# Performance work log

Hardware: AMD Instinct MI355X
Metric: run time of the kernel (lower is better)

Reference implementation:

```python
import jax, jax.numpy as jnp
import numpy as np

R = 32
EPS = 0.0
BN_EPS = 1e-5


def _voxelize(features, idx):
    # features: [C, N], idx: [N] int32 flat voxel index in [0, R^3)
    V = R * R * R
    pts = features.T  # [N, C]
    sums = jax.ops.segment_sum(pts, idx, num_segments=V)          # [V, C]
    cnts = jax.ops.segment_sum(jnp.ones_like(idx, jnp.float32), idx, num_segments=V)  # [V]
    avg = sums / jnp.maximum(cnts, 1.0)[:, None]
    mx = jax.ops.segment_max(pts, idx, num_segments=V)            # [V, C], -inf for empty
    mx = jnp.where(cnts[:, None] > 0, mx, 0.0)
    return avg, mx, cnts


def reference(features, coords, conv_w, conv_b, bn_gamma, bn_beta, bn_mean, bn_var):
    B, C, N = features.shape
    # --- coordinate normalization (coords detached in original) ---
    nc = coords - jnp.mean(coords, axis=2, keepdims=True)          # [B,3,N]
    norms = jnp.linalg.norm(nc, axis=1, keepdims=True)             # [B,1,N]
    denom = jnp.max(norms, axis=2, keepdims=True) * 2.0 + EPS      # [B,1,1]
    nc = nc / denom + 0.5
    nc = jnp.clip(nc * R, 0.0, R - 1)                              # [B,3,N]
    vox = jnp.round(nc).astype(jnp.int32)                          # [B,3,N]
    idx = vox[:, 0] * (R * R) + vox[:, 1] * R + vox[:, 2]          # [B,N]
    # --- dual scatter reduction (avg + max) per batch ---
    avg, mx, _ = jax.vmap(_voxelize)(features, idx)                # [B, V, C] each
    fea = jnp.concatenate([mx, avg], axis=-1)                      # [B, V, 2C]
    # --- 1x1 Conv3d == channel matmul ---
    y = jnp.einsum('bvc,oc->bvo', fea, conv_w) + conv_b            # [B, V, C]
    # --- BatchNorm3d (eval mode) ---
    y = (y - bn_mean) * (bn_gamma / jnp.sqrt(bn_var + BN_EPS)) + bn_beta
    # --- Swish ---
    y = y * jax.nn.sigmoid(y)
    out = jnp.transpose(y, (0, 2, 1)).reshape(B, C, R, R, R)
    return out, nc


def setup_inputs() -> dict:
    key = jax.random.key(0)
    ks = jax.random.split(key, 8)
    B, C, N = 8, 240, 16384
    return {
        'features': jax.random.normal(ks[0], (B, C, N), jnp.float32),
        'coords': jax.random.normal(ks[1], (B, 3, N), jnp.float32),
        'conv_w': jax.random.normal(ks[2], (C, 2 * C), jnp.float32) * 0.05,
        'conv_b': jax.random.normal(ks[3], (C,), jnp.float32) * 0.05,
        'bn_gamma': jnp.ones((C,), jnp.float32),
        'bn_beta': jnp.zeros((C,), jnp.float32),
        'bn_mean': jnp.zeros((C,), jnp.float32),
        'bn_var': jax.random.uniform(ks[4], (C,), jnp.float32, 0.5, 1.5),
    }
```

## Files before the change

### kernel.cpp

```cpp
#include <hip/hip_runtime.h>
#include <math.h>

#define RR 32
#define V 32768
#define C 240
#define N 16384
#define B 8
#define K2C 480
#define NCOL 1024
#define FPAD 488
#define EBUF 512

typedef __attribute__((ext_vector_type(8))) short bf16x8;
typedef __attribute__((ext_vector_type(4))) float f32x4;

__device__ __forceinline__ unsigned short f2bf(float x) {
    unsigned u = __float_as_uint(x);
    u += 0x7fffu + ((u >> 16) & 1u);
    return (unsigned short)(u >> 16);
}
__device__ __forceinline__ float bf2f(unsigned short u) {
    return __uint_as_float(((unsigned)u) << 16);
}

__global__ __launch_bounds__(1024) void stats_kernel(const float* __restrict__ coords,
                                                     float* __restrict__ stats) {
    int b = blockIdx.x, tid = threadIdx.x;
    const float* cb = coords + (size_t)b * 3 * N;
    __shared__ float red[1024];
    float m[3];
    for (int d = 0; d < 3; ++d) {
        float s = 0.f;
        for (int n = tid; n < N; n += 1024) s += cb[d * N + n];
        red[tid] = s; __syncthreads();
        for (int w = 512; w > 0; w >>= 1) { if (tid < w) red[tid] += red[tid + w]; __syncthreads(); }
        m[d] = red[0] / (float)N;
        __syncthreads();
    }
    float mx = 0.f;
    for (int n = tid; n < N; n += 1024) {
        float dx = cb[0 * N + n] - m[0];
        float dy = cb[1 * N + n] - m[1];
        float dz = cb[2 * N + n] - m[2];
        mx = fmaxf(mx, dx * dx + dy * dy + dz * dz);
    }
    red[tid] = mx; __syncthreads();
    for (int w = 512; w > 0; w >>= 1) { if (tid < w) red[tid] = fmaxf(red[tid], red[tid + w]); __syncthreads(); }
    if (tid == 0) {
        stats[b * 4 + 0] = m[0];
        stats[b * 4 + 1] = m[1];
        stats[b * 4 + 2] = m[2];
        stats[b * 4 + 3] = 2.f * sqrtf(red[0]);
    }
}

__global__ __launch_bounds__(256) void nc_idx_kernel(const float* __restrict__ coords,
                                                     const float* __restrict__ stats,
                                                     float* __restrict__ nc_out,
                                                     int* __restrict__ idxbuf,
                                                     int* __restrict__ hist) {
    int t = blockIdx.x * 256 + threadIdx.x;
    int b = t >> 14;
    int n = t & (N - 1);
    float denom = stats[b * 4 + 3];
    int v[3];
#pragma unroll
    for (int d = 0; d < 3; ++d) {
        float x = coords[((size_t)b * 3 + d) * N + n];
        float t0 = (x - stats[b * 4 + d]) / denom + 0.5f;
        t0 = t0 * (float)RR;
        t0 = fminf(fmaxf(t0, 0.f), (float)(RR - 1));
        nc_out[((size_t)b * 3 + d) * N + n] = t0;
        v[d] = (int)rintf(t0);
    }
    int iv = v[0] * (RR * RR) + v[1] * RR + v[2];
    idxbuf[t] = iv;
    atomicAdd(hist + b * V + iv, 1);
}

__global__ __launch_bounds__(1024) void prefix_kernel(const int* __restrict__ hist,
                                                      int* __restrict__ starts,
                                                      int* __restrict__ cursor) {
    __shared__ int part[1024];
    int b = blockIdx.x, t = threadIdx.x;
    int base = b * V + t * 32;
    int s = 0;
    for (int j = 0; j < 32; ++j) s += hist[base + j];
    part[t] = s; __syncthreads();
    for (int off = 1; off < 1024; off <<= 1) {
        int x = (t >= off) ? part[t - off] : 0;
        __syncthreads();
        part[t] += x;
        __syncthreads();
    }
    int run = part[t] - s;
    for (int j = 0; j < 32; ++j) {
        int h = hist[base + j];
        starts[base + j] = run;
        cursor[base + j] = run;
        run += h;
    }
}

__global__ __launch_bounds__(256) void plist_kernel(const int* __restrict__ idxbuf,
                                                    int* __restrict__ cursor,
                                                    int* __restrict__ ptlist) {
    int t = blockIdx.x * 256 + threadIdx.x;
    int b = t >> 14;
    int n = t & (N - 1);
    int iv = idxbuf[t];
    int pos = atomicAdd(cursor + b * V + iv, 1);
    ptlist[(b << 14) + pos] = (n << 5) | (iv & 31);
}

__global__ __launch_bounds__(256) void wcvt_kernel(const float* __restrict__ w,
                                                   unsigned short* __restrict__ w_bf) {
    int i = blockIdx.x * 256 + threadIdx.x;
    w_bf[i] = f2bf(w[i]);
}

__global__ __launch_bounds__(256) void transpose_kernel(const float* __restrict__ feat,
                                                        unsigned short* __restrict__ featT) {
    __shared__ float t[32][33];
    int b = blockIdx.z;
    int n0 = blockIdx.x * 32, c0 = blockIdx.y * 32;
    int l = threadIdx.x;
    int tx = l & 31, ty = l >> 5;
    const float* fb = feat + (size_t)b * C * N;
    unsigned short* fTb = featT + (size_t)b * N * C;
#pragma unroll
    for (int k = 0; k < 4; ++k) {
        int c = c0 + ty + 8 * k;
        if (c < C) t[ty + 8 * k][tx] = fb[(size_t)c * N + n0 + tx];
    }
    __syncthreads();
    int cp = l & 15;
    int nl = l >> 4;
#pragma unroll
    for (int k = 0; k < 2; ++k) {
        int n = n0 + nl + 16 * k;
        int c = c0 + 2 * cp;
        if (c < C) {
            unsigned lo = f2bf(t[2 * cp][nl + 16 * k]);
            unsigned hi = f2bf(t[2 * cp + 1][nl + 16 * k]);
            *(unsigned*)&fTb[(size_t)n * C + c] = lo | (hi << 16);
        }
    }
}

__global__ __launch_bounds__(256) void column_kernel(
    const unsigned short* __restrict__ featT,
    const int* __restrict__ ptlist,
    const int* __restrict__ starts,
    const int* __restrict__ hist,
    const unsigned short* __restrict__ w_bf,
    const float* __restrict__ cbias, const float* __restrict__ gamma,
    const float* __restrict__ beta, const float* __restrict__ mean,
    const float* __restrict__ var,
    float* __restrict__ out) {
    const int col = blockIdx.x, b = blockIdx.y;
    const int tid = threadIdx.x;
    const int v0 = col * 32;
    float* outb = out + (size_t)b * C * V;

    __shared__ float A_s[C], B_s[C];
    __shared__ unsigned short fea_s[32][FPAD];
    __shared__ int cnt_s[32];
    __shared__ int ebuf[EBUF];

    if (tid < C) {
        float sc = gamma[tid] * rsqrtf(var[tid] + 1e-5f);
        A_s[tid] = sc;
        B_s[tid] = (cbias[tid] - mean[tid]) * sc + beta[tid];
    }
    if (tid < 32) cnt_s[tid] = hist[b * V + v0 + tid];
    __syncthreads();

    int pc = 0;
#pragma unroll
    for (int z = 0; z < 32; ++z) pc += cnt_s[z];

    if (pc == 0) {
        for (int i = tid; i < C * 32; i += 256) {
            int o = i >> 5, vv = i & 31;
            float y = B_s[o];
            y = y / (1.f + __expf(-y));
            outb[(size_t)o * V + v0 + vv] = y;
        }
        return;
    }

    for (int i = tid; i < 32 * FPAD / 2; i += 256) ((unsigned*)fea_s)[i] = 0u;

    const int c = (tid < C) ? tid : 0;
    const bool act = tid < C;
    const int pos = starts[b * V + v0];
    const int* pl = ptlist + (b << 14) + pos;
    const unsigned short* fT = featT + (size_t)b * N * C;

    float s = 0.f, mx = -INFINITY;
    int curz = -1;
    for (int base = 0; base < pc; base += EBUF) {
        int mm = min(EBUF, pc - base);
        __syncthreads();
        for (int i = tid; i < mm; i += 256) ebuf[i] = pl[base + i];
        __syncthreads();
        for (int i0 = 0; i0 < mm; i0 += 16) {
            int m = min(16, mm - i0);
            int e_[16];
#pragma unroll
            for (int j = 0; j < 16; ++j) e_[j] = ebuf[i0 + ((j < m) ? j : m - 1)];
            float f_[16];
#pragma unroll
            for (int j = 0; j < 16; ++j) f_[j] = bf2f(fT[(e_[j] >> 5) * C + c]);
#pragma unroll
            for (int j = 0; j < 16; ++j) {
                if (j < m) {
                    int zj = e_[j] & 31;
                    if (zj != curz) {
                        if (curz >= 0 && act) {
                            fea_s[curz][c] = f2bf(mx);
                            fea_s[curz][C + c] = f2bf(s / (float)cnt_s[curz]);
                        }
                        curz = zj; s = 0.f; mx = -INFINITY;
                    }
                    s += f_[j]; mx = fmaxf(mx, f_[j]);
                }
            }
        }
    }
    if (curz >= 0 && act) {
        fea_s[curz][c] = f2bf(mx);
        fea_s[curz][C + c] = f2bf(s / (float)cnt_s[curz]);
    }
    __syncthreads();

    const int lane = tid & 63, wave = tid >> 6;
    const int nt = wave & 1;
    const int mbase = (wave >> 1) * 8;
    const int mcnt = (wave >> 1) ? 7 : 8;
    const int zl = nt * 16 + (lane & 15);
    const int koff = (lane >> 4) * 8;

    f32x4 acc[8];
#pragma unroll
    for (int i = 0; i < 8; ++i) acc[i] = (f32x4){0.f, 0.f, 0.f, 0.f};

#pragma unroll
    for (int kc = 0; kc < 15; ++kc) {
        const int kg = kc * 32 + koff;
        bf16x8 bfr = *(const bf16x8*)&fea_s[zl][kg];
        const unsigned short* wp = w_bf + (size_t)(mbase * 16 + (lane & 15)) * K2C + kg;
#pragma unroll
        for (int mt = 0; mt < 8; ++mt) {
            if (mt < mcnt) {
                bf16x8 afr = *(const bf16x8*)(wp + (size_t)mt * 16 * K2C);
                acc[mt] = __builtin_amdgcn_mfma_f32_16x16x32_bf16(afr, bfr, acc[mt], 0, 0, 0);
            }
        }
    }

    const int vv = v0 + zl;
    const int rbase = (lane >> 4) * 4;
#pragma unroll
    for (int mt = 0; mt < 8; ++mt) {
        if (mt < mcnt) {
#pragma unroll
            for (int r = 0; r < 4; ++r) {
                int o = (mbase + mt) * 16 + rbase + r;
                float y = acc[mt][r] * A_s[o] + B_s[o];
                y = y / (1.f + __expf(-y));
                outb[(size_t)o * V + vv] = y;
            }
        }
    }
}

extern "C" void kernel_launch(void* const* d_in, const int* in_sizes, int n_in,
                              void* d_out, int out_size, void* d_ws, size_t ws_size,
                              hipStream_t stream) {
    const float* features = (const float*)d_in[0];
    const float* coords   = (const float*)d_in[1];
    const float* conv_w   = (const float*)d_in[2];
    const float* conv_b   = (const float*)d_in[3];
    const float* gamma    = (const float*)d_in[4];
    const float* beta     = (const float*)d_in[5];
    const float* mean     = (const float*)d_in[6];
    const float* var      = (const float*)d_in[7];

    float* out    = (float*)d_out;
    float* nc_out = out + (size_t)B * C * V;

    char* ws = (char*)d_ws;
    size_t off = 0;
    auto carve = [&](size_t bytes) { char* p = ws + off; off += (bytes + 255) & ~(size_t)255; return p; };
    int*            hist   = (int*)carve((size_t)B * V * 4);
    float*          stats  = (float*)carve(B * 4 * 4);
    int*            idxbuf = (int*)carve((size_t)B * N * 4);
    int*            starts = (int*)carve((size_t)B * V * 4);
    int*            cursor = (int*)carve((size_t)B * V * 4);
    int*            ptlist = (int*)carve((size_t)B * N * 4);
    unsigned short* w_bf   = (unsigned short*)carve((size_t)C * K2C * 2);
    unsigned short* featT  = (unsigned short*)carve((size_t)B * N * C * 2);
    (void)off;

    hipMemsetAsync(hist, 0, (size_t)B * V * 4, stream);

    stats_kernel<<<B, 1024, 0, stream>>>(coords, stats);
    nc_idx_kernel<<<(B * N) / 256, 256, 0, stream>>>(coords, stats, nc_out, idxbuf, hist);
    prefix_kernel<<<B, 1024, 0, stream>>>(hist, starts, cursor);
    plist_kernel<<<(B * N) / 256, 256, 0, stream>>>(idxbuf, cursor, ptlist);
    wcvt_kernel<<<(C * K2C) / 256, 256, 0, stream>>>(conv_w, w_bf);
    transpose_kernel<<<dim3(N / 32, 8, B), 256, 0, stream>>>(features, featT);
    column_kernel<<<dim3(NCOL, B), 256, 0, stream>>>(
        featT, ptlist, starts, hist, w_bf,
        conv_b, gamma, beta, mean, var, out);
    (void)in_sizes; (void)n_in; (void)out_size;
}
```

Baseline: 648.7 us.

## Fold memset and weight cast into stats kernel; vectorize prefix, transpose, gather

Histogram zeroing and the weight-to-bf16 conversion move into the stats kernel, which removes a memset and a separate launch. The prefix kernel reads and writes histogram counts as int4, and the transpose kernel now handles all 240 channels per block in one larger shared tile. The column gather loads two bf16 channels per thread with 32-bit loads across 120 threads, halving load instructions but leaving more of each wave idle. The changes are spread across several independent kernels.

```diff
diff --git a/kernel.cpp b/kernel.cpp
--- a/kernel.cpp
+++ b/kernel.cpp
@@ -19,13 +19,20 @@
     u += 0x7fffu + ((u >> 16) & 1u);
     return (unsigned short)(u >> 16);
 }
-__device__ __forceinline__ float bf2f(unsigned short u) {
-    return __uint_as_float(((unsigned)u) << 16);
-}
 
 __global__ __launch_bounds__(1024) void stats_kernel(const float* __restrict__ coords,
-                                                     float* __restrict__ stats) {
+                                                     float* __restrict__ stats,
+                                                     int* __restrict__ hist,
+                                                     const float* __restrict__ w,
+                                                     unsigned short* __restrict__ w_bf) {
     int b = blockIdx.x, tid = threadIdx.x;
+    int4 z4 = {0, 0, 0, 0};
+    int4* hz = (int4*)(hist + b * V);
+    for (int i = tid; i < V / 4; i += 1024) hz[i] = z4;
+    for (int i = tid; i < 14400; i += 1024) {
+        int g = b * 14400 + i;
+        w_bf[g] = f2bf(w[g]);
+    }
     const float* cb = coords + (size_t)b * 3 * N;
     __shared__ float red[1024];
     float m[3];
@@ -33,7 +40,7 @@
         float s = 0.f;
         for (int n = tid; n < N; n += 1024) s += cb[d * N + n];
         red[tid] = s; __syncthreads();
-        for (int w = 512; w > 0; w >>= 1) { if (tid < w) red[tid] += red[tid + w]; __syncthreads(); }
+        for (int w2 = 512; w2 > 0; w2 >>= 1) { if (tid < w2) red[tid] += red[tid + w2]; __syncthreads(); }
         m[d] = red[0] / (float)N;
         __syncthreads();
     }
@@ -45,7 +52,7 @@
         mx = fmaxf(mx, dx * dx + dy * dy + dz * dz);
     }
     red[tid] = mx; __syncthreads();
-    for (int w = 512; w > 0; w >>= 1) { if (tid < w) red[tid] = fmaxf(red[tid], red[tid + w]); __syncthreads(); }
+    for (int w2 = 512; w2 > 0; w2 >>= 1) { if (tid < w2) red[tid] = fmaxf(red[tid], red[tid + w2]); __syncthreads(); }
     if (tid == 0) {
         stats[b * 4 + 0] = m[0];
         stats[b * 4 + 1] = m[1];
@@ -84,8 +91,11 @@
     __shared__ int part[1024];
     int b = blockIdx.x, t = threadIdx.x;
     int base = b * V + t * 32;
+    const int4* hp = (const int4*)(hist + base);
+    int4 h[8];
     int s = 0;
-    for (int j = 0; j < 32; ++j) s += hist[base + j];
+#pragma unroll
+    for (int j = 0; j < 8; ++j) { h[j] = hp[j]; s += h[j].x + h[j].y + h[j].z + h[j].w; }
     part[t] = s; __syncthreads();
     for (int off = 1; off < 1024; off <<= 1) {
         int x = (t >= off) ? part[t - off] : 0;
@@ -94,11 +104,16 @@
         __syncthreads();
     }
     int run = part[t] - s;
-    for (int j = 0; j < 32; ++j) {
-        int h = hist[base + j];
-        starts[base + j] = run;
-        cursor[base + j] = run;
-        run += h;
+    int4* sp = (int4*)(starts + base);
+    int4* cp = (int4*)(cursor + base);
+#pragma unroll
+    for (int j = 0; j < 8; ++j) {
+        int4 o;
+        o.x = run; run += h[j].x;
+        o.y = run; run += h[j].y;
+        o.z = run; run += h[j].z;
+        o.w = run; run += h[j].w;
+        sp[j] = o; cp[j] = o;
     }
 }
 
@@ -113,37 +128,30 @@
     ptlist[(b << 14) + pos] = (n << 5) | (iv & 31);
 }
 
-__global__ __launch_bounds__(256) void wcvt_kernel(const float* __restrict__ w,
-                                                   unsigned short* __restrict__ w_bf) {
-    int i = blockIdx.x * 256 + threadIdx.x;
-    w_bf[i] = f2bf(w[i]);
-}
-
 __global__ __launch_bounds__(256) void transpose_kernel(const float* __restrict__ feat,
                                                         unsigned short* __restrict__ featT) {
-    __shared__ float t[32][33];
-    int b = blockIdx.z;
-    int n0 = blockIdx.x * 32, c0 = blockIdx.y * 32;
+    __shared__ float t[C][33];
+    int b = blockIdx.y;
+    int n0 = blockIdx.x * 32;
     int l = threadIdx.x;
-    int tx = l & 31, ty = l >> 5;
     const float* fb = feat + (size_t)b * C * N;
     unsigned short* fTb = featT + (size_t)b * N * C;
-#pragma unroll
-    for (int k = 0; k < 4; ++k) {
-        int c = c0 + ty + 8 * k;
-        if (c < C) t[ty + 8 * k][tx] = fb[(size_t)c * N + n0 + tx];
+    int nl = l & 31, cs = l >> 5;
+#pragma unroll
+    for (int p = 0; p < 30; ++p) {
+        int c = p * 8 + cs;
+        t[c][nl] = fb[(size_t)c * N + n0 + nl];
     }
     __syncthreads();
-    int cp = l & 15;
-    int nl = l >> 4;
-#pragma unroll
-    for (int k = 0; k < 2; ++k) {
-        int n = n0 + nl + 16 * k;
-        int c = c0 + 2 * cp;
-        if (c < C) {
-            unsigned lo = f2bf(t[2 * cp][nl + 16 * k]);
-            unsigned hi = f2bf(t[2 * cp + 1][nl + 16 * k]);
-            *(unsigned*)&fTb[(size_t)n * C + c] = lo | (hi << 16);
+    int ci = l & 127;
+    int nh = l >> 7;
+#pragma unroll
+    for (int p = 0; p < 16; ++p) {
+        int n = 2 * p + nh;
+        if (ci < 120) {
+            unsigned lo = f2bf(t[2 * ci][n]);
+            unsigned hi = f2bf(t[2 * ci + 1][n]);
+            *(unsigned*)&fTb[(size_t)(n0 + n) * C + 2 * ci] = lo | (hi << 16);
         }
     }
 }
@@ -192,46 +200,56 @@
 
     for (int i = tid; i < 32 * FPAD / 2; i += 256) ((unsigned*)fea_s)[i] = 0u;
 
-    const int c = (tid < C) ? tid : 0;
-    const bool act = tid < C;
+    const int cu = tid;
+    const bool act = tid < 120;
     const int pos = starts[b * V + v0];
     const int* pl = ptlist + (b << 14) + pos;
     const unsigned short* fT = featT + (size_t)b * N * C;
 
-    float s = 0.f, mx = -INFINITY;
+    float s0 = 0.f, s1 = 0.f, mx0 = -INFINITY, mx1 = -INFINITY;
     int curz = -1;
     for (int base = 0; base < pc; base += EBUF) {
         int mm = min(EBUF, pc - base);
         __syncthreads();
         for (int i = tid; i < mm; i += 256) ebuf[i] = pl[base + i];
         __syncthreads();
-        for (int i0 = 0; i0 < mm; i0 += 16) {
-            int m = min(16, mm - i0);
-            int e_[16];
-#pragma unroll
-            for (int j = 0; j < 16; ++j) e_[j] = ebuf[i0 + ((j < m) ? j : m - 1)];
-            float f_[16];
-#pragma unroll
-            for (int j = 0; j < 16; ++j) f_[j] = bf2f(fT[(e_[j] >> 5) * C + c]);
-#pragma unroll
-            for (int j = 0; j < 16; ++j) {
-                if (j < m) {
-                    int zj = e_[j] & 31;
-                    if (zj != curz) {
-                        if (curz >= 0 && act) {
-                            fea_s[curz][c] = f2bf(mx);
-                            fea_s[curz][C + c] = f2bf(s / (float)cnt_s[curz]);
+        if (act) {
+            for (int i0 = 0; i0 < mm; i0 += 16) {
+                int m = min(16, mm - i0);
+                int e_[16];
+#pragma unroll
+                for (int j = 0; j < 16; ++j) e_[j] = ebuf[i0 + ((j < m) ? j : m - 1)];
+                unsigned u_[16];
+#pragma unroll
+                for (int j = 0; j < 16; ++j)
+                    u_[j] = *(const unsigned*)&fT[(size_t)(e_[j] >> 5) * C + 2 * cu];
+#pragma unroll
+                for (int j = 0; j < 16; ++j) {
+                    if (j < m) {
+                        int zj = e_[j] & 31;
+                        if (zj != curz) {
+                            if (curz >= 0) {
+                                float k = (float)cnt_s[curz];
+                                unsigned pm = (unsigned)f2bf(mx0) | ((unsigned)f2bf(mx1) << 16);
+                                unsigned pa = (unsigned)f2bf(s0 / k) | ((unsigned)f2bf(s1 / k) << 16);
+                                *(unsigned*)&fea_s[curz][2 * cu] = pm;
+                                *(unsigned*)&fea_s[curz][C + 2 * cu] = pa;
+                            }
+                            curz = zj; s0 = s1 = 0.f; mx0 = mx1 = -INFINITY;
                         }
-                        curz = zj; s = 0.f; mx = -INFINITY;
+                        float lo = __uint_as_float(u_[j] << 16);
+                        float hi = __uint_as_float(u_[j] & 0xffff0000u);
+                        s0 += lo; s1 += hi;
+                        mx0 = fmaxf(mx0, lo); mx1 = fmaxf(mx1, hi);
                     }
-                    s += f_[j]; mx = fmaxf(mx, f_[j]);
                 }
             }
         }
     }
-    if (curz >= 0 && act) {
-        fea_s[curz][c] = f2bf(mx);
-        fea_s[curz][C + c] = f2bf(s / (float)cnt_s[curz]);
+    if (act && curz >= 0) {
+        float k = (float)cnt_s[curz];
+        *(unsigned*)&fea_s[curz][2 * cu] = (unsigned)f2bf(mx0) | ((unsigned)f2bf(mx1) << 16);
+        *(unsigned*)&fea_s[curz][C + 2 * cu] = (unsigned)f2bf(s0 / k) | ((unsigned)f2bf(s1 / k) << 16);
     }
     __syncthreads();
 
@@ -304,14 +322,11 @@
     unsigned short* featT  = (unsigned short*)carve((size_t)B * N * C * 2);
     (void)off;
 
-    hipMemsetAsync(hist, 0, (size_t)B * V * 4, stream);
-
-    stats_kernel<<<B, 1024, 0, stream>>>(coords, stats);
+    stats_kernel<<<B, 1024, 0, stream>>>(coords, stats, hist, conv_w, w_bf);
     nc_idx_kernel<<<(B * N) / 256, 256, 0, stream>>>(coords, stats, nc_out, idxbuf, hist);
     prefix_kernel<<<B, 1024, 0, stream>>>(hist, starts, cursor);
     plist_kernel<<<(B * N) / 256, 256, 0, stream>>>(idxbuf, cursor, ptlist);
-    wcvt_kernel<<<(C * K2C) / 256, 256, 0, stream>>>(conv_w, w_bf);
-    transpose_kernel<<<dim3(N / 32, 8, B), 256, 0, stream>>>(features, featT);
+    transpose_kernel<<<dim3(N / 32, B), 256, 0, stream>>>(features, featT);
     column_kernel<<<dim3(NCOL, B), 256, 0, stream>>>(
         featT, ptlist, starts, hist, w_bf,
         conv_b, gamma, beta, mean, var, out);
```

After: 639.8 us. Within noise of the previous version (-1.4%).
